# Performance work log

Hardware: AMD Instinct MI355X
Metric: run time of the kernel (lower is better)

## Reference

```python
import jax, jax.numpy as jnp
import numpy as np

N = 100000       # nodes
E = 1600000      # edges (avg degree 16)
F_IN = 128
F_OUT = 128
EPS = 1e-5       # GraphNorm eps
NEG_SLOPE = 0.01 # nn.LeakyReLU default


def setup_inputs() -> dict:
    key = jax.random.key(0)
    ks = jax.random.split(key, 4)
    x = jax.random.normal(ks[0], (N, F_IN), dtype=jnp.float32)
    edge_index = jax.random.randint(ks[1], (2, E), 0, N, dtype=jnp.int64)
    # GCNConv linear weight (stored as [in, out] for x @ W)
    W = jax.random.normal(ks[2], (F_IN, F_OUT), dtype=jnp.float32) / np.sqrt(F_IN).astype(np.float32)
    b = jnp.zeros((F_OUT,), jnp.float32)          # GCNConv bias
    gn_weight = jnp.ones((F_OUT,), jnp.float32)   # GraphNorm weight
    gn_bias = jnp.zeros((F_OUT,), jnp.float32)    # GraphNorm bias
    gn_mean_scale = jnp.ones((F_OUT,), jnp.float32)  # GraphNorm mean_scale
    return {"x": x, "edge_index": edge_index, "W": W, "b": b,
            "gn_weight": gn_weight, "gn_bias": gn_bias, "gn_mean_scale": gn_mean_scale}


def reference(x, edge_index, W, b, gn_weight, gn_bias, gn_mean_scale):
    n = x.shape[0]
    # --- GCNConv with add_self_loops=True, symmetric normalization ---
    loops = jnp.arange(n, dtype=edge_index.dtype)
    src = jnp.concatenate([edge_index[0], loops])  # [E+N]
    dst = jnp.concatenate([edge_index[1], loops])  # [E+N]
    deg = jax.ops.segment_sum(jnp.ones(src.shape, x.dtype), dst, num_segments=n)  # [N]
    deg_inv_sqrt = jnp.where(deg > 0, 1.0 / jnp.sqrt(deg), 0.0)
    norm = deg_inv_sqrt[src] * deg_inv_sqrt[dst]   # [E+N]
    h = x @ W                                      # [N, F_OUT]
    agg = jax.ops.segment_sum(h[src] * norm[:, None], dst, num_segments=n) + b  # [N, F_OUT]
    # --- GraphNorm (single graph: stats over all nodes, per-feature) ---
    mean = jnp.mean(agg, axis=0)                   # [F_OUT]
    centered = agg - mean * gn_mean_scale
    var = jnp.mean(centered * centered, axis=0)
    out = centered / jnp.sqrt(var + EPS) * gn_weight + gn_bias
    # --- LeakyReLU ---
    out = jnp.where(out > 0, out, NEG_SLOPE * out)
    return (out, edge_index)
```

## Files before the change

### kernel.cpp

```cpp
#include <hip/hip_runtime.h>

#define NN 100000
#define NE 1600000
#define F  128

#define SH   8
#define NPB  256
#define NBKT 391
#define B1   256
#define CH1  6250
#define MATN (NBKT * B1)
#define MATP (98 * 1024)
#define BCAP2 6144

#define SB   256

constexpr float EPS   = 1e-5f;
constexpr float SLOPE = 0.01f;

typedef __attribute__((ext_vector_type(8))) short short8;
typedef __attribute__((ext_vector_type(4))) float f32x4;
typedef __attribute__((ext_vector_type(2))) float f32x2;

__device__ inline unsigned int bf16rne(float f) {
    unsigned int u = __float_as_uint(f);
    return (u + 0x7fffu + ((u >> 16) & 1u)) >> 16;
}
__device__ inline unsigned int pack2(float a, float b) {
    return bf16rne(a) | (bf16rne(b) << 16);
}
__device__ inline f32x2 pkadd(f32x2 a, f32x2 b) {
    f32x2 d;
    asm("v_pk_add_f32 %0, %1, %2" : "=v"(d) : "v"(a), "v"(b));
    return d;
}
__device__ inline f32x2 pkfma(f32x2 a, f32x2 b, f32x2 c) {
    f32x2 d;
    asm("v_pk_fma_f32 %0, %1, %2, %3" : "=v"(d) : "v"(a), "v"(b), "v"(c));
    return d;
}
__device__ inline f32x2 fp8lo(unsigned int u) {
    return __builtin_amdgcn_cvt_pk_f32_fp8(u, false);
}
__device__ inline f32x2 fp8hi(unsigned int u) {
    return __builtin_amdgcn_cvt_pk_f32_fp8(u, true);
}
__device__ inline unsigned int fp8pack4(float a, float b, float c, float d) {
    int o = 0;
    o = __builtin_amdgcn_cvt_pk_fp8_f32(a, b, o, false);
    o = __builtin_amdgcn_cvt_pk_fp8_f32(c, d, o, true);
    return (unsigned int)o;
}

__global__ __launch_bounds__(1024) void k_hist1(const int* __restrict__ dst,
                                                unsigned int* __restrict__ mat,
                                                const float* __restrict__ Wm,
                                                unsigned int* __restrict__ Wt) {
    __shared__ unsigned int h[NBKT];
    if (threadIdx.x < NBKT) h[threadIdx.x] = 0u;
    __syncthreads();
    if (blockIdx.x < 8) {
        int idx = blockIdx.x * 1024 + threadIdx.x;
        int p = idx & 3, lane = (idx >> 2) & 63, n = (idx >> 8) & 7, kk = idx >> 11;
        int k0 = kk * 32 + (lane >> 4) * 8 + 2 * p;
        int c  = n * 16 + (lane & 15);
        unsigned int lo = bf16rne(Wm[k0 * F + c]);
        unsigned int hi = bf16rne(Wm[(k0 + 1) * F + c]);
        Wt[idx] = lo | (hi << 16);
    }
    const int e0 = blockIdx.x * CH1;
    for (int i = threadIdx.x; i < CH1; i += 1024)
        atomicAdd(&h[dst[e0 + i] >> SH], 1u);
    __syncthreads();
    if (threadIdx.x < NBKT) mat[threadIdx.x * B1 + blockIdx.x] = h[threadIdx.x];
}

__global__ __launch_bounds__(1024) void k_scanA(const unsigned int* __restrict__ mat,
                                                unsigned int* __restrict__ scn,
                                                unsigned int* __restrict__ bsums) {
    __shared__ unsigned int ps[1024];
    const int t = threadIdx.x;
    const int i = blockIdx.x * 1024 + t;
    unsigned int v = mat[i];
    ps[t] = v;
    __syncthreads();
    for (int off = 1; off < 1024; off <<= 1) {
        unsigned int a = (t >= off) ? ps[t - off] : 0u;
        __syncthreads();
        ps[t] += a;
        __syncthreads();
    }
    scn[i] = ps[t];
    if (t == 1023) bsums[blockIdx.x] = ps[1023];
}


__global__ __launch_bounds__(1024) void k_scat1(const int* __restrict__ ei,
                                                const unsigned int* __restrict__ mat,
                                                const unsigned int* __restrict__ scn,
                                                const unsigned int* __restrict__ bsums,
                                                unsigned int* __restrict__ ebuf) {
    __shared__ unsigned int cur[NBKT];
    __shared__ unsigned int bo[128];
    const int t = threadIdx.x;
    if (t < 128) {
        unsigned int v = (t < 98) ? bsums[t] : 0u;
        bo[t] = v;
        for (int off = 1; off < 128; off <<= 1) {
            __syncthreads();
            unsigned int a = (t >= off) ? bo[t - off] : 0u;
            __syncthreads();
            bo[t] += a;
        }
        bo[t] -= v;
    } else {
        for (int off = 1; off < 128; off <<= 1) { __syncthreads(); __syncthreads(); }
    }
    __syncthreads();
    if (t < NBKT) {
        int idx = t * B1 + blockIdx.x;
        cur[t] = scn[idx] + bo[idx >> 10] - mat[idx];
    }
    __syncthreads();
    const int e0 = blockIdx.x * CH1;
    for (int i = t; i < CH1; i += 1024) {
        int s = ei[e0 + i];
        int d = ei[NE + e0 + i];
        unsigned int pos = atomicAdd(&cur[d >> SH], 1u);
        ebuf[pos] = ((unsigned int)(d & (NPB - 1)) << 17) | (unsigned int)s;
    }
}

__global__ __launch_bounds__(256) void k_fill2(const unsigned int* __restrict__ mat,
                                               const unsigned int* __restrict__ scn,
                                               const unsigned int* __restrict__ bsums,
                                               const unsigned int* __restrict__ ebuf,
                                               int* __restrict__ row_start,
                                               float* __restrict__ dis,
                                               int* __restrict__ csr) {
    __shared__ unsigned int stage[BCAP2];
    __shared__ unsigned int hist[NPB];
    __shared__ unsigned int cur[NPB];
    __shared__ unsigned int ps[NPB];
    __shared__ unsigned int bo[128];
    const int t = threadIdx.x;
    const int bkt = blockIdx.x;
    hist[t] = 0u;
    if (t < 128) {
        unsigned int v = (t < 98) ? bsums[t] : 0u;
        bo[t] = v;
        for (int off = 1; off < 128; off <<= 1) {
            __syncthreads();
            unsigned int a = (t >= off) ? bo[t - off] : 0u;
            __syncthreads();
            bo[t] += a;
        }
        bo[t] -= v;
    } else {
        for (int off = 1; off < 128; off <<= 1) { __syncthreads(); __syncthreads(); }
    }
    __syncthreads();
    const int i0 = bkt * B1;
    const unsigned int ebase = scn[i0] + bo[i0 >> 10] - mat[i0];
    unsigned int eend;
    if (bkt == NBKT - 1) eend = (unsigned int)NE;
    else {
        const int i1 = (bkt + 1) * B1;
        eend = scn[i1] + bo[i1 >> 10] - mat[i1];
    }
    const unsigned int n = eend - ebase;
    const unsigned int m = (n < BCAP2) ? n : BCAP2;
    for (unsigned int i = t; i < m; i += 256) {
        unsigned int v = ebuf[ebase + i];
        stage[i] = v;
        atomicAdd(&hist[v >> 17], 1u);
    }
    for (unsigned int i = BCAP2 + t; i < n; i += 256)
        atomicAdd(&hist[ebuf[ebase + i] >> 17], 1u);
    __syncthreads();
    const unsigned int deg = hist[t];
    ps[t] = deg;
    __syncthreads();
    for (int off = 1; off < 256; off <<= 1) {
        unsigned int a = (t >= off) ? ps[t - off] : 0u;
        __syncthreads();
        ps[t] += a;
        __syncthreads();
    }
    const unsigned int ex = (t == 0) ? 0u : ps[t - 1];
    cur[t] = ebase + ex;
    const int node = bkt * NPB + t;
    if (node <= NN) row_start[node] = (int)(ebase + ex);
    if (node < NN)  dis[node] = rsqrtf((float)(deg + 1u));
    __syncthreads();
    for (unsigned int i = t; i < m; i += 256) {
        unsigned int v = stage[i];
        unsigned int pos = atomicAdd(&cur[v >> 17], 1u);
        csr[pos] = (int)(v & 0x1FFFFu);
    }
    for (unsigned int i = BCAP2 + t; i < n; i += 256) {
        unsigned int v = ebuf[ebase + i];
        unsigned int pos = atomicAdd(&cur[v >> 17], 1u);
        csr[pos] = (int)(v & 0x1FFFFu);
    }
}

__global__ __launch_bounds__(256) void k_gemm(const float* __restrict__ x,
                                              const unsigned int* __restrict__ Wt,
                                              const float* __restrict__ dis,
                                              unsigned int* __restrict__ g32) {
    __shared__ unsigned int xl[128 * 64];
    const int tid = threadIdx.x;
    const int lane = tid & 63, wave = tid >> 6;
    const int row0 = blockIdx.x * 128;

#pragma unroll
    for (int i = 0; i < 16; ++i) {
        int fi = i * 256 + tid;
        int lr = fi >> 5;
        int cf = (fi & 31) * 4;
        int gr = row0 + lr; if (gr >= NN) gr = NN - 1;
        float4 v = *(const float4*)(x + (size_t)gr * F + cf);
        unsigned int u0 = pack2(v.x, v.y);
        unsigned int u1 = pack2(v.z, v.w);
        int cu = (cf >> 1) ^ ((lr & 7) << 2);
        uint2 w2; w2.x = u0; w2.y = u1;
        *(uint2*)&xl[lr * 64 + cu] = w2;
    }
    __syncthreads();

    const int rbase = row0 + wave * 32;
    short8 afr[2][4];
#pragma unroll
    for (int m = 0; m < 2; ++m) {
        int lr = wave * 32 + m * 16 + (lane & 15);
#pragma unroll
        for (int kk = 0; kk < 4; ++kk) {
            int cu = (kk * 16 + (lane >> 4) * 4) ^ ((lr & 7) << 2);
            afr[m][kk] = *(const short8*)&xl[lr * 64 + cu];
        }
    }

    f32x4 acc[2][8];
#pragma unroll
    for (int m = 0; m < 2; ++m)
#pragma unroll
        for (int n = 0; n < 8; ++n) { f32x4 z = {0.f, 0.f, 0.f, 0.f}; acc[m][n] = z; }

    const uint4* Wt4 = (const uint4*)Wt;
#pragma unroll
    for (int kk = 0; kk < 4; ++kk) {
        union { uint4 u; short8 s; } bfr[8];
#pragma unroll
        for (int n = 0; n < 8; ++n) bfr[n].u = Wt4[(kk * 8 + n) * 64 + lane];
#pragma unroll
        for (int m = 0; m < 2; ++m)
#pragma unroll
            for (int n = 0; n < 8; ++n)
                acc[m][n] = __builtin_amdgcn_mfma_f32_16x16x32_bf16(bfr[n].s, afr[m][kk], acc[m][n], 0, 0, 0);
    }

#pragma unroll
    for (int m = 0; m < 2; ++m) {
        int xr = rbase + m * 16 + (lane & 15);
        bool ok = xr < NN;
        float d = ok ? dis[xr] : 0.0f;
        unsigned int* gp = g32 + (size_t)(ok ? xr : 0) * 32 + (lane >> 4);
#pragma unroll
        for (int n = 0; n < 8; ++n) {
            unsigned int w = fp8pack4(acc[m][n][0] * d, acc[m][n][1] * d,
                                      acc[m][n][2] * d, acc[m][n][3] * d);
            if (ok) gp[n * 4] = w;
        }
    }
}

__global__ __launch_bounds__(256) void k_gather(const unsigned int* __restrict__ g32,
                                                const int* __restrict__ csr,
                                                const int* __restrict__ row_start,
                                                const float* __restrict__ dis,
                                                const float* __restrict__ b,
                                                unsigned int* __restrict__ agg8) {
    const int lane = threadIdx.x & 63;
    const int node = blockIdx.x * 4 + (threadIdx.x >> 6);
    if (node >= NN) return;
    const int q = lane >> 4;
    const int c = lane & 15;
    const int j = row_start[node];
    const int e = row_start[node + 1];
    const int L = e - j + 1;
    int sv = (j + lane < e) ? csr[j + lane] : node;
    f32x2 A0 = {0.f, 0.f}, A1 = A0, A2 = A0, A3 = A0;
    int k = 0;
    const int L1 = (L < 64) ? L : 64;
    for (; k < L1; k += 16) {
        int k0 = k + q, k1 = k0 + 4, k2 = k0 + 8, k3 = k0 + 12;
        int r0 = __shfl(sv, k0);
        int r1 = __shfl(sv, k1);
        int r2 = __shfl(sv, k2);
        int r3 = __shfl(sv, k3);
        bool p0 = k0 < L, p1 = k1 < L, p2 = k2 < L, p3 = k3 < L;
        uint2 v0, v1, v2, v3;
        if (p0) v0 = *(const uint2*)&g32[(size_t)r0 * 32 + c * 2];
        if (p1) v1 = *(const uint2*)&g32[(size_t)r1 * 32 + c * 2];
        if (p2) v2 = *(const uint2*)&g32[(size_t)r2 * 32 + c * 2];
        if (p3) v3 = *(const uint2*)&g32[(size_t)r3 * 32 + c * 2];
        if (p0) {
            A0 = pkadd(A0, fp8lo(v0.x)); A1 = pkadd(A1, fp8hi(v0.x));
            A2 = pkadd(A2, fp8lo(v0.y)); A3 = pkadd(A3, fp8hi(v0.y));
        }
        if (p1) {
            A0 = pkadd(A0, fp8lo(v1.x)); A1 = pkadd(A1, fp8hi(v1.x));
            A2 = pkadd(A2, fp8lo(v1.y)); A3 = pkadd(A3, fp8hi(v1.y));
        }
        if (p2) {
            A0 = pkadd(A0, fp8lo(v2.x)); A1 = pkadd(A1, fp8hi(v2.x));
            A2 = pkadd(A2, fp8lo(v2.y)); A3 = pkadd(A3, fp8hi(v2.y));
        }
        if (p3) {
            A0 = pkadd(A0, fp8lo(v3.x)); A1 = pkadd(A1, fp8hi(v3.x));
            A2 = pkadd(A2, fp8lo(v3.y)); A3 = pkadd(A3, fp8hi(v3.y));
        }
    }
    for (; k < L; k += 16) {
#pragma unroll
        for (int s = 0; s < 4; ++s) {
            int ks = k + q + s * 4;
            if (ks < L) {
                int rs = (j + ks < e) ? csr[j + ks] : node;
                uint2 v = *(const uint2*)&g32[(size_t)rs * 32 + c * 2];
                A0 = pkadd(A0, fp8lo(v.x)); A1 = pkadd(A1, fp8hi(v.x));
                A2 = pkadd(A2, fp8lo(v.y)); A3 = pkadd(A3, fp8hi(v.y));
            }
        }
    }
#define RED2(A) A.x += __shfl_xor(A.x, 16); A.x += __shfl_xor(A.x, 32); \
                A.y += __shfl_xor(A.y, 16); A.y += __shfl_xor(A.y, 32);
    RED2(A0) RED2(A1) RED2(A2) RED2(A3)
#undef RED2
    if (q == 0) {
        float d = dis[node];
        const float4* bp = (const float4*)&b[c * 8];
        float4 b0 = bp[0], b1 = bp[1];
        uint2 w;
        w.x = fp8pack4(b0.x + d * A0.x, b0.y + d * A0.y,
                       b0.z + d * A1.x, b0.w + d * A1.y);
        w.y = fp8pack4(b1.x + d * A2.x, b1.y + d * A2.y,
                       b1.z + d * A3.x, b1.w + d * A3.y);
        *(uint2*)&agg8[(size_t)node * 32 + c * 2] = w;
    }
}

__global__ __launch_bounds__(256) void k_stats(const unsigned int* __restrict__ agg8,
                                               float* __restrict__ partials) {
    __shared__ float lds[4][8][32];
    const int tid = threadIdx.x;
    const int lane = tid & 63, wave = tid >> 6;
    const uint4* a4 = (const uint4*)agg8;
    const long total  = (long)NN * 8;
    const long stride = (long)SB * 256;
    f32x2 S[8], Q[8];
#pragma unroll
    for (int i = 0; i < 8; ++i) { f32x2 z = {0.f, 0.f}; S[i] = z; Q[i] = z; }
    for (long i = (long)blockIdx.x * 256 + tid; i < total; i += stride) {
        uint4 v = a4[i];
        f32x2 p0 = fp8lo(v.x), p1 = fp8hi(v.x), p2 = fp8lo(v.y), p3 = fp8hi(v.y);
        f32x2 p4 = fp8lo(v.z), p5 = fp8hi(v.z), p6 = fp8lo(v.w), p7 = fp8hi(v.w);
        S[0] = pkadd(S[0], p0); Q[0] = pkfma(p0, p0, Q[0]);
        S[1] = pkadd(S[1], p1); Q[1] = pkfma(p1, p1, Q[1]);
        S[2] = pkadd(S[2], p2); Q[2] = pkfma(p2, p2, Q[2]);
        S[3] = pkadd(S[3], p3); Q[3] = pkfma(p3, p3, Q[3]);
        S[4] = pkadd(S[4], p4); Q[4] = pkfma(p4, p4, Q[4]);
        S[5] = pkadd(S[5], p5); Q[5] = pkfma(p5, p5, Q[5]);
        S[6] = pkadd(S[6], p6); Q[6] = pkfma(p6, p6, Q[6]);
        S[7] = pkadd(S[7], p7); Q[7] = pkfma(p7, p7, Q[7]);
    }
#pragma unroll
    for (int i = 0; i < 8; ++i) {
        S[i].x += __shfl_xor(S[i].x, 8); S[i].x += __shfl_xor(S[i].x, 16); S[i].x += __shfl_xor(S[i].x, 32);
        S[i].y += __shfl_xor(S[i].y, 8); S[i].y += __shfl_xor(S[i].y, 16); S[i].y += __shfl_xor(S[i].y, 32);
        Q[i].x += __shfl_xor(Q[i].x, 8); Q[i].x += __shfl_xor(Q[i].x, 16); Q[i].x += __shfl_xor(Q[i].x, 32);
        Q[i].y += __shfl_xor(Q[i].y, 8); Q[i].y += __shfl_xor(Q[i].y, 16); Q[i].y += __shfl_xor(Q[i].y, 32);
    }
    if (lane < 8) {
#pragma unroll
        for (int i = 0; i < 8; ++i) {
            lds[wave][lane][2 * i]      = S[i].x;
            lds[wave][lane][2 * i + 1]  = S[i].y;
            lds[wave][lane][16 + 2 * i]     = Q[i].x;
            lds[wave][lane][16 + 2 * i + 1] = Q[i].y;
        }
    }
    __syncthreads();
    const int kind = tid >> 7;
    const int f = tid & 127;
    const int l = f >> 4, slot = (f & 15) + 16 * kind;
    float v = lds[0][l][slot] + lds[1][l][slot] + lds[2][l][slot] + lds[3][l][slot];
    partials[(size_t)blockIdx.x * 256 + tid] = v;
}

__global__ __launch_bounds__(256) void k_red(const float* __restrict__ partials,
                                             float* __restrict__ stats) {
    float a0 = 0.f, a1 = 0.f, a2 = 0.f, a3 = 0.f;
    for (int bq = 0; bq < SB; bq += 4) {
        a0 += partials[(bq + 0) * 256 + threadIdx.x];
        a1 += partials[(bq + 1) * 256 + threadIdx.x];
        a2 += partials[(bq + 2) * 256 + threadIdx.x];
        a3 += partials[(bq + 3) * 256 + threadIdx.x];
    }
    stats[threadIdx.x] = (a0 + a1) + (a2 + a3);
}

__global__ __launch_bounds__(256) void k_normei(const unsigned int* __restrict__ agg8,
                                               const float* __restrict__ stats,
                                               const float* __restrict__ gw,
                                               const float* __restrict__ gb,
                                               const float* __restrict__ gms,
                                               float* __restrict__ out0,
                                               const int* __restrict__ ei,
                                               float* __restrict__ out1) {
    __shared__ float A[F], Bc[F];
    if (threadIdx.x < F) {
        int f = threadIdx.x;
        const float invn = 1.0f / (float)NN;
        float mean = stats[f] * invn;
        float ms = mean * gms[f];
        float var = stats[F + f] * invn - 2.0f * ms * mean + ms * ms;
        float inv = rsqrtf(var + EPS);
        float a = inv * gw[f];
        A[f] = a;
        Bc[f] = gb[f] - ms * a;
    }
    __syncthreads();
    const int c8 = threadIdx.x & 7;
    float ra[16], rb[16];
#pragma unroll
    for (int i = 0; i < 16; ++i) { ra[i] = A[c8 * 16 + i]; rb[i] = Bc[c8 * 16 + i]; }
    const uint4* a4 = (const uint4*)agg8;
    const int4* ei4 = (const int4*)ei;
    float4* o14 = (float4*)out1;
    const long total  = (long)NN * 8;
    const long stride = (long)gridDim.x * 256;
    for (long i = (long)blockIdx.x * 256 + threadIdx.x; i < total; i += stride) {
        uint4 v = a4[i];
        f32x2 p0 = fp8lo(v.x), p1 = fp8hi(v.x), p2 = fp8lo(v.y), p3 = fp8hi(v.y);
        f32x2 p4 = fp8lo(v.z), p5 = fp8hi(v.z), p6 = fp8lo(v.w), p7 = fp8hi(v.w);
        float fv[16];
        fv[0] = p0.x * ra[0] + rb[0];   fv[1] = p0.y * ra[1] + rb[1];
        fv[2] = p1.x * ra[2] + rb[2];   fv[3] = p1.y * ra[3] + rb[3];
        fv[4] = p2.x * ra[4] + rb[4];   fv[5] = p2.y * ra[5] + rb[5];
        fv[6] = p3.x * ra[6] + rb[6];   fv[7] = p3.y * ra[7] + rb[7];
        fv[8] = p4.x * ra[8] + rb[8];   fv[9] = p4.y * ra[9] + rb[9];
        fv[10] = p5.x * ra[10] + rb[10]; fv[11] = p5.y * ra[11] + rb[11];
        fv[12] = p6.x * ra[12] + rb[12]; fv[13] = p6.y * ra[13] + rb[13];
        fv[14] = p7.x * ra[14] + rb[14]; fv[15] = p7.y * ra[15] + rb[15];
#pragma unroll
        for (int t = 0; t < 16; ++t) fv[t] = fv[t] > 0.f ? fv[t] : SLOPE * fv[t];
        float* op = out0 + i * 16;
#pragma unroll
        for (int t = 0; t < 4; ++t) {
            float4 r; r.x = fv[4 * t]; r.y = fv[4 * t + 1]; r.z = fv[4 * t + 2]; r.w = fv[4 * t + 3];
            *(float4*)(op + 4 * t) = r;
        }
        int4 ev = ei4[i];
        unsigned int z;
        asm("v_and_b32 %0, 0, %1" : "=v"(z) : "v"(v.x));
        float4 r;
        r.x = (float)(ev.x | (int)z);
        r.y = (float)ev.y;
        r.z = (float)ev.z;
        r.w = (float)ev.w;
        o14[i] = r;
    }
}

extern "C" void kernel_launch(void* const* d_in, const int* in_sizes, int n_in,
                              void* d_out, int out_size, void* d_ws, size_t ws_size,
                              hipStream_t stream) {
    const float* x   = (const float*)d_in[0];
    const int*   ei  = (const int*)d_in[1];
    const float* Wm  = (const float*)d_in[2];
    const float* b   = (const float*)d_in[3];
    const float* gw  = (const float*)d_in[4];
    const float* gb  = (const float*)d_in[5];
    const float* gms = (const float*)d_in[6];

    float* out  = (float*)d_out;
    float* out1 = out + (size_t)NN * F;
    unsigned int* agg8 = (unsigned int*)out1;

    unsigned int* wsu   = (unsigned int*)d_ws;
    unsigned int* g32   = wsu;
    unsigned int* ebuf  = wsu;
    unsigned int* mat   = g32 + (size_t)NN * 32;
    unsigned int* scn   = mat + MATP;
    unsigned int* bsums = scn + MATP;
    int* row_start      = (int*)(bsums + 128);
    int* csr            = row_start + NN + 2;
    float* dis          = (float*)(csr + NE + 8);
    float* stats        = dis + NN;
    unsigned int* Wt    = (unsigned int*)(stats + 256);
    float* partials     = (float*)(Wt + 8192);

    k_hist1<<<B1, 1024, 0, stream>>>(ei + NE, mat, Wm, Wt);
    k_scanA<<<98, 1024, 0, stream>>>(mat, scn, bsums);
    k_scat1<<<B1, 1024, 0, stream>>>(ei, mat, scn, bsums, ebuf);
    k_fill2<<<NBKT, 256, 0, stream>>>(mat, scn, bsums, ebuf, row_start, dis, csr);
    k_gemm<<<(NN + 127) / 128, 256, 0, stream>>>(x, Wt, dis, g32);
    k_gather<<<NN / 4, 256, 0, stream>>>(g32, csr, row_start, dis, b, agg8);
    k_stats<<<SB, 256, 0, stream>>>(agg8, partials);
    k_red<<<1, 256, 0, stream>>>(partials, stats);
    k_normei<<<2048, 256, 0, stream>>>(agg8, stats, gw, gb, gms, out, ei, out1);
}
```

Measured before the change: 136.1 us.

## Fuse stats reduction into last block, split histogram bins, enlarge gather blocks

The separate single-block reduction kernel is removed. The last k_stats block to finish, found through an atomic counter with thread fences, now sums the per-block partials, which saves one kernel launch. The histogram kernel splits its shared-memory bins across two copies by wave parity to cut atomic contention, and resets the counter. The gather kernel moves from 256-thread to 512-thread blocks, handling 8 nodes per block. These changes remove a launch gap and some contention, but add fence and atomic overhead.

```diff
diff --git a/kernel.cpp b/kernel.cpp
--- a/kernel.cpp
+++ b/kernel.cpp
@@ -55,12 +55,14 @@
 __global__ __launch_bounds__(1024) void k_hist1(const int* __restrict__ dst,
                                                 unsigned int* __restrict__ mat,
                                                 const float* __restrict__ Wm,
-                                                unsigned int* __restrict__ Wt) {
-    __shared__ unsigned int h[NBKT];
-    if (threadIdx.x < NBKT) h[threadIdx.x] = 0u;
+                                                unsigned int* __restrict__ Wt,
+                                                unsigned int* __restrict__ done) {
+    __shared__ unsigned int h[2][NBKT];
+    const int t = threadIdx.x;
+    if (t < NBKT) { h[0][t] = 0u; h[1][t] = 0u; }
     __syncthreads();
     if (blockIdx.x < 8) {
-        int idx = blockIdx.x * 1024 + threadIdx.x;
+        int idx = blockIdx.x * 1024 + t;
         int p = idx & 3, lane = (idx >> 2) & 63, n = (idx >> 8) & 7, kk = idx >> 11;
         int k0 = kk * 32 + (lane >> 4) * 8 + 2 * p;
         int c  = n * 16 + (lane & 15);
@@ -68,11 +70,13 @@
         unsigned int hi = bf16rne(Wm[(k0 + 1) * F + c]);
         Wt[idx] = lo | (hi << 16);
     }
+    if (blockIdx.x == 8 && t == 0) done[0] = 0u;
+    const int par = (t >> 6) & 1;
     const int e0 = blockIdx.x * CH1;
-    for (int i = threadIdx.x; i < CH1; i += 1024)
-        atomicAdd(&h[dst[e0 + i] >> SH], 1u);
-    __syncthreads();
-    if (threadIdx.x < NBKT) mat[threadIdx.x * B1 + blockIdx.x] = h[threadIdx.x];
+    for (int i = t; i < CH1; i += 1024)
+        atomicAdd(&h[par][dst[e0 + i] >> SH], 1u);
+    __syncthreads();
+    if (t < NBKT) mat[t * B1 + blockIdx.x] = h[0][t] + h[1][t];
 }
 
 __global__ __launch_bounds__(1024) void k_scanA(const unsigned int* __restrict__ mat,
@@ -275,14 +279,14 @@
     }
 }
 
-__global__ __launch_bounds__(256) void k_gather(const unsigned int* __restrict__ g32,
+__global__ __launch_bounds__(512) void k_gather(const unsigned int* __restrict__ g32,
                                                 const int* __restrict__ csr,
                                                 const int* __restrict__ row_start,
                                                 const float* __restrict__ dis,
                                                 const float* __restrict__ b,
                                                 unsigned int* __restrict__ agg8) {
     const int lane = threadIdx.x & 63;
-    const int node = blockIdx.x * 4 + (threadIdx.x >> 6);
+    const int node = blockIdx.x * 8 + (threadIdx.x >> 6);
     if (node >= NN) return;
     const int q = lane >> 4;
     const int c = lane & 15;
@@ -352,8 +356,11 @@
 }
 
 __global__ __launch_bounds__(256) void k_stats(const unsigned int* __restrict__ agg8,
-                                               float* __restrict__ partials) {
+                                               float* __restrict__ partials,
+                                               float* __restrict__ stats,
+                                               unsigned int* __restrict__ done) {
     __shared__ float lds[4][8][32];
+    __shared__ unsigned int isLast;
     const int tid = threadIdx.x;
     const int lane = tid & 63, wave = tid >> 6;
     const uint4* a4 = (const uint4*)agg8;
@@ -392,23 +399,31 @@
         }
     }
     __syncthreads();
-    const int kind = tid >> 7;
-    const int f = tid & 127;
-    const int l = f >> 4, slot = (f & 15) + 16 * kind;
-    float v = lds[0][l][slot] + lds[1][l][slot] + lds[2][l][slot] + lds[3][l][slot];
-    partials[(size_t)blockIdx.x * 256 + tid] = v;
-}
-
-__global__ __launch_bounds__(256) void k_red(const float* __restrict__ partials,
-                                             float* __restrict__ stats) {
-    float a0 = 0.f, a1 = 0.f, a2 = 0.f, a3 = 0.f;
-    for (int bq = 0; bq < SB; bq += 4) {
-        a0 += partials[(bq + 0) * 256 + threadIdx.x];
-        a1 += partials[(bq + 1) * 256 + threadIdx.x];
-        a2 += partials[(bq + 2) * 256 + threadIdx.x];
-        a3 += partials[(bq + 3) * 256 + threadIdx.x];
-    }
-    stats[threadIdx.x] = (a0 + a1) + (a2 + a3);
+    {
+        const int kind = tid >> 7;
+        const int f = tid & 127;
+        const int l = f >> 4, slot = (f & 15) + 16 * kind;
+        float v = lds[0][l][slot] + lds[1][l][slot] + lds[2][l][slot] + lds[3][l][slot];
+        partials[(size_t)blockIdx.x * 256 + tid] = v;
+    }
+    __syncthreads();
+    if (tid == 0) {
+        __threadfence();
+        unsigned int old = atomicAdd(done, 1u);
+        isLast = (old == SB - 1) ? 1u : 0u;
+    }
+    __syncthreads();
+    if (isLast) {
+        __threadfence();
+        float a0 = 0.f, a1 = 0.f, a2 = 0.f, a3 = 0.f;
+        for (int bq = 0; bq < SB; bq += 4) {
+            a0 += partials[(bq + 0) * 256 + tid];
+            a1 += partials[(bq + 1) * 256 + tid];
+            a2 += partials[(bq + 2) * 256 + tid];
+            a3 += partials[(bq + 3) * 256 + tid];
+        }
+        stats[tid] = (a0 + a1) + (a2 + a3);
+    }
 }
 
 __global__ __launch_bounds__(256) void k_normei(const unsigned int* __restrict__ agg8,
@@ -500,15 +515,15 @@
     float* dis          = (float*)(csr + NE + 8);
     float* stats        = dis + NN;
     unsigned int* Wt    = (unsigned int*)(stats + 256);
-    float* partials     = (float*)(Wt + 8192);
-
-    k_hist1<<<B1, 1024, 0, stream>>>(ei + NE, mat, Wm, Wt);
+    unsigned int* done  = Wt + 8192;
+    float* partials     = (float*)(done + 64);
+
+    k_hist1<<<B1, 1024, 0, stream>>>(ei + NE, mat, Wm, Wt, done);
     k_scanA<<<98, 1024, 0, stream>>>(mat, scn, bsums);
     k_scat1<<<B1, 1024, 0, stream>>>(ei, mat, scn, bsums, ebuf);
     k_fill2<<<NBKT, 256, 0, stream>>>(mat, scn, bsums, ebuf, row_start, dis, csr);
     k_gemm<<<(NN + 127) / 128, 256, 0, stream>>>(x, Wt, dis, g32);
-    k_gather<<<NN / 4, 256, 0, stream>>>(g32, csr, row_start, dis, b, agg8);
-    k_stats<<<SB, 256, 0, stream>>>(agg8, partials);
-    k_red<<<1, 256, 0, stream>>>(partials, stats);
+    k_gather<<<NN / 8, 512, 0, stream>>>(g32, csr, row_start, dis, b, agg8);
+    k_stats<<<SB, 256, 0, stream>>>(agg8, partials, stats, done);
     k_normei<<<2048, 256, 0, stream>>>(agg8, stats, gw, gb, gms, out, ei, out1);
 }
```

After: 143.5 us. 1.05x slower.
